# Kernel optimization log

Measured on AMD Instinct MI355X. Metric: run time of the kernel, lower is better.

## Reference

```python
import jax, jax.numpy as jnp
import numpy as np

B, S, DIM = 4, 2048, 512
HEADS, DHEAD = 8, 64
INNER = HEADS * DHEAD


def setup_inputs() -> dict:
    key = jax.random.key(0)
    k1, k2, k3, k4 = jax.random.split(key, 4)
    x = jax.random.normal(k1, (B, S, DIM), dtype=jnp.float32)
    W_qkv = jax.random.normal(k2, (DIM, 3 * INNER), dtype=jnp.float32) * (DIM ** -0.5)
    W_out = jax.random.normal(k3, (INNER, DIM), dtype=jnp.float32) * (INNER ** -0.5)
    b_out = jnp.zeros((DIM,), dtype=jnp.float32)
    # learnable log-temperature, initialized to log(dim_head**-0.5)
    log_temp = jnp.asarray(np.log(DHEAD ** -0.5), dtype=jnp.float32)
    return {"x": x, "W_qkv": W_qkv, "log_temp": log_temp, "W_out": W_out, "b_out": b_out}


def reference(x, W_qkv, log_temp, W_out, b_out):
    b, s, _ = x.shape
    qkv = x @ W_qkv  # [b, s, 3*inner]
    q, k, v = jnp.split(qkv, 3, axis=-1)
    # [b, s, inner] -> [b, h, s, d]
    reshape = lambda t: t.reshape(b, s, HEADS, DHEAD).transpose(0, 2, 1, 3)
    q, k, v = reshape(q), reshape(k), reshape(v)
    dots = jnp.einsum("bhid,bhjd->bhij", q, k) * jnp.exp(log_temp)
    mask_value = -jnp.finfo(dots.dtype).max
    eye = jnp.eye(s, dtype=bool)
    dots = jnp.where(eye, mask_value, dots)
    attn = jax.nn.softmax(dots, axis=-1)
    out = jnp.einsum("bhij,bhjd->bhid", attn, v)
    out = out.transpose(0, 2, 1, 3).reshape(b, s, INNER)
    return out @ W_out + b_out
```

## Files before the change

### kernel.cpp

```cpp
#include <hip/hip_runtime.h>
#include <hip/hip_bf16.h>

#define BB 4
#define SS 2048
#define DIMM 512
#define HH 8
#define DD 64
#define NQKV 1536

typedef float  floatx4 __attribute__((ext_vector_type(4)));
typedef short  bf16x8  __attribute__((ext_vector_type(8)));
typedef short  bf16x4  __attribute__((ext_vector_type(4)));

#define MFMA16(A, B, C) __builtin_amdgcn_mfma_f32_16x16x32_bf16(A, B, C, 0, 0, 0)

__device__ __forceinline__ unsigned short f2bf(float f) {
    unsigned int u = __float_as_uint(f);
    u += 0x7FFFu + ((u >> 16) & 1u);
    return (unsigned short)(u >> 16);
}

__device__ __forceinline__ unsigned int f2bf_pk(float lo, float hi) {
    float2 f; f.x = lo; f.y = hi;
    __hip_bfloat162 h = __float22bfloat162_rn(f);
    return *reinterpret_cast<unsigned int*>(&h);
}

__device__ __forceinline__ float fast_exp2(float x) {
#if __has_builtin(__builtin_amdgcn_exp2f)
    return __builtin_amdgcn_exp2f(x);
#else
    return __exp2f(x);
#endif
}

__device__ __forceinline__ void gl_lds16(const void* g, void* l) {
    __builtin_amdgcn_global_load_lds(
        (__attribute__((address_space(1))) void*)g,
        (__attribute__((address_space(3))) void*)l,
        16, 0, 0);
}

__global__ __launch_bounds__(256) void k_prep(
    const float* __restrict__ x, const float* __restrict__ W_qkv,
    const float* __restrict__ W_out,
    unsigned short* __restrict__ xb, unsigned short* __restrict__ Wq_t,
    unsigned short* __restrict__ Wo_t) {
    __shared__ float t[32][33];
    int bid = blockIdx.x, tid = threadIdx.x;
    if (bid < 4096) {
        int i = (bid * 256 + tid) * 4;
        float4 v = *(const float4*)(x + i);
        ushort4 o;
        o.x = f2bf(v.x); o.y = f2bf(v.y); o.z = f2bf(v.z); o.w = f2bf(v.w);
        *(ushort4*)(xb + i) = o;
        return;
    }
    const float* in; unsigned short* out; int R = 512, C, bx, by;
    if (bid < 4864) { in = W_qkv; out = Wq_t; C = 1536; int blk = bid - 4096; bx = blk % 48; by = blk / 48; }
    else            { in = W_out; out = Wo_t; C = 512;  int blk = bid - 4864; bx = blk % 16; by = blk / 16; }
    int tx = tid & 31, ty = tid >> 5;
    int c0 = bx * 32, r0 = by * 32;
    for (int i = 0; i < 4; i++) {
        int r = r0 + ty + i * 8;
        t[ty + i * 8][tx] = in[(size_t)r * C + c0 + tx];
    }
    __syncthreads();
    for (int i = 0; i < 4; i++) {
        int cc = c0 + ty + i * 8;
        out[(size_t)cc * R + r0 + tx] = f2bf(t[tx][ty + i * 8]);
    }
}

__global__ __launch_bounds__(256) void k_gemm_qkv(
    const unsigned short* __restrict__ A,
    const unsigned short* __restrict__ Bt,
    const float* __restrict__ log_temp,
    unsigned short* __restrict__ Qb,
    unsigned short* __restrict__ Kb,
    unsigned short* __restrict__ Vt) {
    __shared__ unsigned short smem[2][128 * 64];
    unsigned short* As = smem[0];
    unsigned short* Bs = smem[1];
    const int K = 512;
    int bid = blockIdx.x;
    int swz = (bid & 7) * 96 + (bid >> 3);
    int local = swz % 96;
    int m_blk = (swz / 96) * 8 + (local & 7);
    int n_blk = local >> 3;
    int m0 = m_blk * 128, n0 = n_blk * 128;
    int tid = threadIdx.x;
    int w = tid >> 6, lane = tid & 63;
    int c = lane & 15, q4 = lane >> 4;
    int wm = w >> 1, wn = w & 1;
    float qscale = __expf(log_temp[0]) * 1.44269504f;

    floatx4 acc[4][4] = {};

    for (int k0 = 0; k0 < K; k0 += 64) {
        __syncthreads();
        for (int i = 0; i < 4; i++) {
            int cidx = w * 256 + i * 64 + lane;
            int row = cidx >> 3, cc = cidx & 7;
            int gcc = cc ^ (row & 7);
            gl_lds16(A + (size_t)(m0 + row) * K + k0 + gcc * 8,
                     As + (size_t)(w * 256 + i * 64) * 8);
            gl_lds16(Bt + (size_t)(n0 + row) * K + k0 + gcc * 8,
                     Bs + (size_t)(w * 256 + i * 64) * 8);
        }
        __syncthreads();
        bf16x8 aF[2][4], bF[2][4];
        for (int kh = 0; kh < 2; kh++)
            for (int mt = 0; mt < 4; mt++) {
                int row = wm * 64 + mt * 16 + c;
                aF[kh][mt] = *(const bf16x8*)&As[row * 64 + (((kh * 4 + q4) ^ (row & 7)) * 8)];
            }
        for (int kh = 0; kh < 2; kh++)
            for (int nt = 0; nt < 4; nt++) {
                int row = wn * 64 + nt * 16 + c;
                bF[kh][nt] = *(const bf16x8*)&Bs[row * 64 + (((kh * 4 + q4) ^ (row & 7)) * 8)];
            }
        for (int kh = 0; kh < 2; kh++)
            for (int mt = 0; mt < 4; mt++)
                for (int nt = 0; nt < 4; nt++)
                    acc[mt][nt] = MFMA16(aF[kh][mt], bF[kh][nt], acc[mt][nt]);
    }

    if (n0 < 1024) {
        for (int nt = 0; nt < 4; nt++) {
            int n = n0 + wn * 64 + nt * 16 + c;
            int t = n >> 9, inner = n & 511;
            int h = inner >> 6, d = inner & 63;
            for (int mt = 0; mt < 4; mt++) {
                for (int r = 0; r < 4; r++) {
                    int m = m0 + wm * 64 + mt * 16 + q4 * 4 + r;
                    int b = m >> 11, s = m & 2047;
                    int bh = b * 8 + h;
                    float v = acc[mt][nt][r];
                    if (t == 0)  Qb[((size_t)bh * SS + s) * 64 + d] = f2bf(v * qscale);
                    else         Kb[((size_t)bh * SS + s) * 64 + d] = f2bf(v);
                }
            }
        }
    } else {
        unsigned short* T = &smem[0][0];
        int b = m0 >> 11, s_base = m0 & 2047;
        for (int half = 0; half < 2; half++) {
            __syncthreads();
            if (wn == half) {
                for (int nt = 0; nt < 4; nt++)
                    for (int mt = 0; mt < 4; mt++)
                        for (int r = 0; r < 4; r++)
                            T[(nt * 16 + c) * 136 + wm * 64 + mt * 16 + q4 * 4 + r] =
                                f2bf(acc[mt][nt][r]);
            }
            __syncthreads();
            for (int rr = 0; rr < 4; rr++) {
                int nl = w * 16 + rr * 4 + q4;
                int ml = c * 8;
                bf16x8 v = *(const bf16x8*)&T[nl * 136 + ml];
                int n = n0 + half * 64 + nl;
                int h = (n >> 6) - 16, d = n & 63;
                int bh = b * 8 + h;
                *(bf16x8*)(Vt + ((size_t)bh * 64 + d) * SS + s_base + ml) = v;
            }
        }
    }
}

__global__ __launch_bounds__(512, 4) void k_attn(
    const unsigned short* __restrict__ Qb,
    const unsigned short* __restrict__ Kb,
    const unsigned short* __restrict__ Vt,
    unsigned short* __restrict__ AO) {
    __shared__ unsigned short KVs[2][2][2][64 * 64];
    int bid = blockIdx.x;
    int swz = (bid & 7) * 64 + (bid >> 3);
    int q0 = (swz & 15) * 128;
    int bh = swz >> 4;
    int h = bh & 7, b = bh >> 3;
    int tid = threadIdx.x, w = tid >> 6, lane = tid & 63;
    int wg = w >> 2, wi = w & 3;
    int c = lane & 15, q4 = lane >> 4;

    const unsigned short* Kbase = Kb + (size_t)bh * SS * 64 + (size_t)wg * 1024 * 64;
    const unsigned short* Vbase = Vt + (size_t)bh * 64 * SS;

    bf16x8 qf[2][2];
    for (int mt = 0; mt < 2; mt++) {
        const unsigned short* qp = Qb + ((size_t)bh * SS + q0 + wi * 32 + mt * 16 + c) * 64;
        qf[mt][0] = *(const bf16x8*)(qp + q4 * 8);
        qf[mt][1] = *(const bf16x8*)(qp + 32 + q4 * 8);
    }
    bf16x8 ones;
    for (int i = 0; i < 8; i++) ones[i] = (short)0x3F80;

    int cidx0 = wi * 128 + lane, cidx1 = cidx0 + 64;
    int row0 = cidx0 >> 3, cc0 = cidx0 & 7;
    int row1 = cidx1 >> 3, cc1 = cidx1 & 7;
    int fk0 = (row0 & 3) | ((row0 >> 1) & 4);
    int fk1 = (row1 & 3) | ((row1 >> 1) & 4);
    const unsigned short* ksrc0 = Kbase + (size_t)row0 * 64 + (cc0 ^ fk0) * 8;
    const unsigned short* ksrc1 = Kbase + (size_t)row1 * 64 + (cc1 ^ fk1) * 8;
    const unsigned short* vsrc0 = Vbase + (size_t)row0 * SS + wg * 1024 + (cc0 ^ (row0 & 7)) * 8;
    const unsigned short* vsrc1 = Vbase + (size_t)row1 * SS + wg * 1024 + (cc1 ^ (row1 & 7)) * 8;
    unsigned short* kdst0 = &KVs[0][wg][0][0] + wi * 1024;
    unsigned short* kdst1 = kdst0 + 512;
    unsigned short* vdst0 = &KVs[1][wg][0][0] + wi * 1024;
    unsigned short* vdst1 = vdst0 + 512;

    gl_lds16(ksrc0, kdst0); gl_lds16(ksrc1, kdst1);
    gl_lds16(vsrc0, vdst0); gl_lds16(vsrc1, vdst1);

    int mask_j0 = (q0 + wi * 32) & ~63;
    int mglob0 = q0 + wi * 32 + c;
    int mglob1 = mglob0 + 16;
    floatx4 oacc[2][4] = {};
    floatx4 osum[2] = {};

    for (int jt = 0; jt < 16; jt++) {
        int buf = jt & 1;
        int j0 = wg * 1024 + jt * 64;
        __syncthreads();
        if (jt + 1 < 16) {
            int jl = (jt + 1) * 64;
            gl_lds16(ksrc0 + (size_t)jl * 64, kdst0 + (buf ^ 1) * 4096);
            gl_lds16(ksrc1 + (size_t)jl * 64, kdst1 + (buf ^ 1) * 4096);
            gl_lds16(vsrc0 + jl, vdst0 + (buf ^ 1) * 4096);
            gl_lds16(vsrc1 + jl, vdst1 + (buf ^ 1) * 4096);
        }
        bool diag = (j0 == mask_j0);
        const unsigned short* Ksb = &KVs[0][wg][buf][0];
        const unsigned short* Vsb = &KVs[1][wg][buf][0];

        for (int g = 0; g < 2; g++) {
            bf16x8 kf[2][2];
            for (int inner = 0; inner < 2; inner++) {
                int row = g * 32 + ((c >> 2) << 3) + inner * 4 + (c & 3);
                kf[inner][0] = *(const bf16x8*)&Ksb[row * 64 + ((q4 ^ (c & 7)) * 8)];
                kf[inner][1] = *(const bf16x8*)&Ksb[row * 64 + (((4 + q4) ^ (c & 7)) * 8)];
            }
            bf16x8 vf[4];
            for (int dt = 0; dt < 4; dt++) {
                int vrow = dt * 16 + c;
                vf[dt] = *(const bf16x8*)&Vsb[vrow * 64 + (((g * 4 + q4) ^ (c & 7)) * 8)];
            }

            floatx4 sa[2][2];
            __builtin_amdgcn_s_setprio(1);
            for (int mt = 0; mt < 2; mt++)
                for (int inner = 0; inner < 2; inner++) {
                    floatx4 t = {};
                    t = MFMA16(kf[inner][0], qf[mt][0], t);
                    t = MFMA16(kf[inner][1], qf[mt][1], t);
                    sa[mt][inner] = t;
                }
            __builtin_amdgcn_s_setprio(0);

            if (diag) {
                for (int inner = 0; inner < 2; inner++)
                    for (int r = 0; r < 4; r++) {
                        int jg = j0 + g * 32 + q4 * 8 + inner * 4 + r;
                        if (jg == mglob0) sa[0][inner][r] = -1e30f;
                        if (jg == mglob1) sa[1][inner][r] = -1e30f;
                    }
            }

            for (int mt = 0; mt < 2; mt++) {
                float e0 = fast_exp2(sa[mt][0][0]), e1 = fast_exp2(sa[mt][0][1]);
                float e2 = fast_exp2(sa[mt][0][2]), e3 = fast_exp2(sa[mt][0][3]);
                float e4 = fast_exp2(sa[mt][1][0]), e5 = fast_exp2(sa[mt][1][1]);
                float e6 = fast_exp2(sa[mt][1][2]), e7 = fast_exp2(sa[mt][1][3]);
                union { bf16x8 v; unsigned int u[4]; } P;
                P.u[0] = f2bf_pk(e0, e1); P.u[1] = f2bf_pk(e2, e3);
                P.u[2] = f2bf_pk(e4, e5); P.u[3] = f2bf_pk(e6, e7);
                __builtin_amdgcn_s_setprio(1);
                for (int dt = 0; dt < 4; dt++)
                    oacc[mt][dt] = MFMA16(P.v, vf[dt], oacc[mt][dt]);
                osum[mt] = MFMA16(P.v, ones, osum[mt]);
                __builtin_amdgcn_s_setprio(0);
            }
        }
    }

    __syncthreads();
    float* p = (float*)&KVs[0][0][0][0] + ((size_t)(wi * 64 + lane)) * 41;
    if (wg == 1) {
        for (int mt = 0; mt < 2; mt++)
            for (int dt = 0; dt < 4; dt++)
                for (int r = 0; r < 4; r++)
                    p[mt * 16 + dt * 4 + r] = oacc[mt][dt][r];
        for (int mt = 0; mt < 2; mt++)
            for (int r = 0; r < 4; r++)
                p[32 + mt * 4 + r] = osum[mt][r];
    }
    __syncthreads();
    if (wg == 0) {
        for (int mt = 0; mt < 2; mt++)
            for (int dt = 0; dt < 4; dt++)
                for (int r = 0; r < 4; r++)
                    oacc[mt][dt][r] += p[mt * 16 + dt * 4 + r];
        for (int mt = 0; mt < 2; mt++)
            for (int r = 0; r < 4; r++)
                osum[mt][r] += p[32 + mt * 4 + r];

        for (int mt = 0; mt < 2; mt++) {
            for (int r = 0; r < 4; r++) {
                float inv = 1.0f / osum[mt][r];
                int s = q0 + wi * 32 + mt * 16 + q4 * 4 + r;
                for (int dt = 0; dt < 4; dt++)
                    AO[((size_t)b * SS + s) * 512 + h * 64 + dt * 16 + c] =
                        f2bf(oacc[mt][dt][r] * inv);
            }
        }
    }
}

__global__ __launch_bounds__(256) void k_gemm_out(
    const unsigned short* __restrict__ A,
    const unsigned short* __restrict__ Bt,
    const float* __restrict__ bias,
    float* __restrict__ out) {
    __shared__ unsigned short As[64 * 64];
    __shared__ unsigned short Bs[128 * 64];
    const int K = 512;
    int m0 = blockIdx.x * 64, n0 = blockIdx.y * 128;
    int tid = threadIdx.x;
    int w = tid >> 6, lane = tid & 63;
    int c = lane & 15, q4 = lane >> 4;

    floatx4 acc[8] = {};

    for (int k0 = 0; k0 < K; k0 += 64) {
        __syncthreads();
        for (int i = 0; i < 2; i++) {
            int cidx = i * 256 + tid;
            int row = cidx >> 3, cc = cidx & 7;
            int gcc = cc ^ (row & 7);
            gl_lds16(A + (size_t)(m0 + row) * K + k0 + gcc * 8,
                     As + (size_t)(i * 256 + w * 64) * 8);
        }
        for (int i = 0; i < 4; i++) {
            int cidx = i * 256 + tid;
            int row = cidx >> 3, cc = cidx & 7;
            int gcc = cc ^ (row & 7);
            gl_lds16(Bt + (size_t)(n0 + row) * K + k0 + gcc * 8,
                     Bs + (size_t)(i * 256 + w * 64) * 8);
        }
        __syncthreads();
        bf16x8 aF[2], bF[2][8];
        for (int kh = 0; kh < 2; kh++) {
            int row = w * 16 + c;
            aF[kh] = *(const bf16x8*)&As[row * 64 + (((kh * 4 + q4) ^ (row & 7)) * 8)];
        }
        for (int kh = 0; kh < 2; kh++)
            for (int nt = 0; nt < 8; nt++) {
                int row = nt * 16 + c;
                bF[kh][nt] = *(const bf16x8*)&Bs[row * 64 + (((kh * 4 + q4) ^ (row & 7)) * 8)];
            }
        for (int kh = 0; kh < 2; kh++)
            for (int nt = 0; nt < 8; nt++)
                acc[nt] = MFMA16(aF[kh], bF[kh][nt], acc[nt]);
    }

    for (int nt = 0; nt < 8; nt++) {
        int n = n0 + nt * 16 + c;
        float bv = bias[n];
        for (int r = 0; r < 4; r++) {
            int m = m0 + w * 16 + q4 * 4 + r;
            out[(size_t)m * 512 + n] = acc[nt][r] + bv;
        }
    }
}

extern "C" void kernel_launch(void* const* d_in, const int* in_sizes, int n_in,
                              void* d_out, int out_size, void* d_ws, size_t ws_size,
                              hipStream_t stream) {
    const float* x        = (const float*)d_in[0];
    const float* W_qkv    = (const float*)d_in[1];
    const float* log_temp = (const float*)d_in[2];
    const float* W_out    = (const float*)d_in[3];
    const float* b_out    = (const float*)d_in[4];
    float* out = (float*)d_out;

    char* ws = (char*)d_ws;
    unsigned short* xb   = (unsigned short*)(ws + 0);
    unsigned short* Wq_t = (unsigned short*)(ws + 8388608);
    unsigned short* Wo_t = (unsigned short*)(ws + 9961472);
    unsigned short* Qb   = (unsigned short*)(ws + 10485760);
    unsigned short* Kb   = (unsigned short*)(ws + 18874368);
    unsigned short* Vt   = (unsigned short*)(ws + 27262976);
    unsigned short* AO   = (unsigned short*)(ws + 35651584);

    k_prep<<<5120, 256, 0, stream>>>(x, W_qkv, W_out, xb, Wq_t, Wo_t);
    k_gemm_qkv<<<768, 256, 0, stream>>>(xb, Wq_t, log_temp, Qb, Kb, Vt);
    k_attn<<<512, 512, 0, stream>>>(Qb, Kb, Vt, AO);
    k_gemm_out<<<dim3(128, 4), 256, 0, stream>>>(AO, Wo_t, b_out, out);
}
```

Baseline: 149.5 us.

## Software-pipeline attention QK^T with previous group's softmax-PV; drop QKV GEMM block swizzle

The attention inner loop now computes the QK^T scores for the next 32-key group before running the exp and PV MFMAs of the previous group, carrying that group's scores and V fragments across tile iterations. The goal is to overlap score MFMAs with the exp/convert VALU work and LDS reads, so the MFMA unit is not left waiting on dependent chains. The price is extra live registers for the carried state, which could lower occupancy. Separately, the QKV GEMM drops its grid swizzle for a plain 2D grid, which may weaken L2 reuse of the A and B tiles.

Measured after the change: 177.8 us. +18.9%, slower.

```diff
diff --git a/kernel.cpp b/kernel.cpp
--- a/kernel.cpp
+++ b/kernel.cpp
@@ -83,12 +83,7 @@
     unsigned short* As = smem[0];
     unsigned short* Bs = smem[1];
     const int K = 512;
-    int bid = blockIdx.x;
-    int swz = (bid & 7) * 96 + (bid >> 3);
-    int local = swz % 96;
-    int m_blk = (swz / 96) * 8 + (local & 7);
-    int n_blk = local >> 3;
-    int m0 = m_blk * 128, n0 = n_blk * 128;
+    int m0 = blockIdx.x * 128, n0 = blockIdx.y * 128;
     int tid = threadIdx.x;
     int w = tid >> 6, lane = tid & 63;
     int c = lane & 15, q4 = lane >> 4;
@@ -194,6 +189,7 @@
     }
     bf16x8 ones;
     for (int i = 0; i < 8; i++) ones[i] = (short)0x3F80;
+    const floatx4 fzero = {};
 
     int cidx0 = wi * 128 + lane, cidx1 = cidx0 + 64;
     int row0 = cidx0 >> 3, cc0 = cidx0 & 7;
@@ -218,6 +214,56 @@
     floatx4 oacc[2][4] = {};
     floatx4 osum[2] = {};
 
+    floatx4 saP[2][2];
+    bf16x8 vfP[4];
+
+    auto qkt_part = [&](const unsigned short* Ksb, int j0, int g, floatx4 (&sa)[2][2]) {
+        bf16x8 kf[2][2];
+        for (int inner = 0; inner < 2; inner++) {
+            int row = g * 32 + ((c >> 2) << 3) + inner * 4 + (c & 3);
+            kf[inner][0] = *(const bf16x8*)&Ksb[row * 64 + ((q4 ^ (c & 7)) * 8)];
+            kf[inner][1] = *(const bf16x8*)&Ksb[row * 64 + (((4 + q4) ^ (c & 7)) * 8)];
+        }
+        __builtin_amdgcn_s_setprio(1);
+        for (int mt = 0; mt < 2; mt++)
+            for (int inner = 0; inner < 2; inner++) {
+                floatx4 t = MFMA16(kf[inner][0], qf[mt][0], fzero);
+                t = MFMA16(kf[inner][1], qf[mt][1], t);
+                sa[mt][inner] = t;
+            }
+        __builtin_amdgcn_s_setprio(0);
+        if (j0 == mask_j0) {
+            for (int inner = 0; inner < 2; inner++)
+                for (int r = 0; r < 4; r++) {
+                    int jg = j0 + g * 32 + q4 * 8 + inner * 4 + r;
+                    if (jg == mglob0) sa[0][inner][r] = -1e30f;
+                    if (jg == mglob1) sa[1][inner][r] = -1e30f;
+                }
+        }
+    };
+    auto load_vf = [&](const unsigned short* Vsb, int g, bf16x8 (&vf)[4]) {
+        for (int dt = 0; dt < 4; dt++) {
+            int vrow = dt * 16 + c;
+            vf[dt] = *(const bf16x8*)&Vsb[vrow * 64 + (((g * 4 + q4) ^ (c & 7)) * 8)];
+        }
+    };
+    auto epv = [&](const floatx4 (&sa)[2][2], const bf16x8 (&vf)[4]) {
+        for (int mt = 0; mt < 2; mt++) {
+            float e0 = fast_exp2(sa[mt][0][0]), e1 = fast_exp2(sa[mt][0][1]);
+            float e2 = fast_exp2(sa[mt][0][2]), e3 = fast_exp2(sa[mt][0][3]);
+            float e4 = fast_exp2(sa[mt][1][0]), e5 = fast_exp2(sa[mt][1][1]);
+            float e6 = fast_exp2(sa[mt][1][2]), e7 = fast_exp2(sa[mt][1][3]);
+            union { bf16x8 v; unsigned int u[4]; } P;
+            P.u[0] = f2bf_pk(e0, e1); P.u[1] = f2bf_pk(e2, e3);
+            P.u[2] = f2bf_pk(e4, e5); P.u[3] = f2bf_pk(e6, e7);
+            __builtin_amdgcn_s_setprio(1);
+            for (int dt = 0; dt < 4; dt++)
+                oacc[mt][dt] = MFMA16(P.v, vf[dt], oacc[mt][dt]);
+            osum[mt] = MFMA16(P.v, ones, osum[mt]);
+            __builtin_amdgcn_s_setprio(0);
+        }
+    };
+
     for (int jt = 0; jt < 16; jt++) {
         int buf = jt & 1;
         int j0 = wg * 1024 + jt * 64;
@@ -229,59 +275,19 @@
             gl_lds16(vsrc0 + jl, vdst0 + (buf ^ 1) * 4096);
             gl_lds16(vsrc1 + jl, vdst1 + (buf ^ 1) * 4096);
         }
-        bool diag = (j0 == mask_j0);
         const unsigned short* Ksb = &KVs[0][wg][buf][0];
         const unsigned short* Vsb = &KVs[1][wg][buf][0];
 
-        for (int g = 0; g < 2; g++) {
-            bf16x8 kf[2][2];
-            for (int inner = 0; inner < 2; inner++) {
-                int row = g * 32 + ((c >> 2) << 3) + inner * 4 + (c & 3);
-                kf[inner][0] = *(const bf16x8*)&Ksb[row * 64 + ((q4 ^ (c & 7)) * 8)];
-                kf[inner][1] = *(const bf16x8*)&Ksb[row * 64 + (((4 + q4) ^ (c & 7)) * 8)];
-            }
-            bf16x8 vf[4];
-            for (int dt = 0; dt < 4; dt++) {
-                int vrow = dt * 16 + c;
-                vf[dt] = *(const bf16x8*)&Vsb[vrow * 64 + (((g * 4 + q4) ^ (c & 7)) * 8)];
-            }
-
-            floatx4 sa[2][2];
-            __builtin_amdgcn_s_setprio(1);
-            for (int mt = 0; mt < 2; mt++)
-                for (int inner = 0; inner < 2; inner++) {
-                    floatx4 t = {};
-                    t = MFMA16(kf[inner][0], qf[mt][0], t);
-                    t = MFMA16(kf[inner][1], qf[mt][1], t);
-                    sa[mt][inner] = t;
-                }
-            __builtin_amdgcn_s_setprio(0);
-
-            if (diag) {
-                for (int inner = 0; inner < 2; inner++)
-                    for (int r = 0; r < 4; r++) {
-                        int jg = j0 + g * 32 + q4 * 8 + inner * 4 + r;
-                        if (jg == mglob0) sa[0][inner][r] = -1e30f;
-                        if (jg == mglob1) sa[1][inner][r] = -1e30f;
-                    }
-            }
-
-            for (int mt = 0; mt < 2; mt++) {
-                float e0 = fast_exp2(sa[mt][0][0]), e1 = fast_exp2(sa[mt][0][1]);
-                float e2 = fast_exp2(sa[mt][0][2]), e3 = fast_exp2(sa[mt][0][3]);
-                float e4 = fast_exp2(sa[mt][1][0]), e5 = fast_exp2(sa[mt][1][1]);
-                float e6 = fast_exp2(sa[mt][1][2]), e7 = fast_exp2(sa[mt][1][3]);
-                union { bf16x8 v; unsigned int u[4]; } P;
-                P.u[0] = f2bf_pk(e0, e1); P.u[1] = f2bf_pk(e2, e3);
-                P.u[2] = f2bf_pk(e4, e5); P.u[3] = f2bf_pk(e6, e7);
-                __builtin_amdgcn_s_setprio(1);
-                for (int dt = 0; dt < 4; dt++)
-                    oacc[mt][dt] = MFMA16(P.v, vf[dt], oacc[mt][dt]);
-                osum[mt] = MFMA16(P.v, ones, osum[mt]);
-                __builtin_amdgcn_s_setprio(0);
-            }
-        }
-    }
+        floatx4 saA[2][2];
+        bf16x8 vfA[4];
+        qkt_part(Ksb, j0, 0, saA);
+        load_vf(Vsb, 0, vfA);
+        if (jt) epv(saP, vfP);
+        qkt_part(Ksb, j0, 1, saP);
+        load_vf(Vsb, 1, vfP);
+        epv(saA, vfA);
+    }
+    epv(saP, vfP);
 
     __syncthreads();
     float* p = (float*)&KVs[0][0][0][0] + ((size_t)(wi * 64 + lane)) * 41;
@@ -393,7 +399,7 @@
     unsigned short* AO   = (unsigned short*)(ws + 35651584);
 
     k_prep<<<5120, 256, 0, stream>>>(x, W_qkv, W_out, xb, Wq_t, Wo_t);
-    k_gemm_qkv<<<768, 256, 0, stream>>>(xb, Wq_t, log_temp, Qb, Kb, Vt);
+    k_gemm_qkv<<<dim3(64, 12), 256, 0, stream>>>(xb, Wq_t, log_temp, Qb, Kb, Vt);
     k_attn<<<512, 512, 0, stream>>>(Qb, Kb, Vt, AO);
     k_gemm_out<<<dim3(128, 4), 256, 0, stream>>>(AO, Wo_t, b_out, out);
 }
```
